# Optimization experiments

Measured on AMD Instinct MI355X. Metric: run time of the kernel, lower is better.

Reference implementation:

```python
import jax, jax.numpy as jnp
import numpy as np

N_NODES = 100000
N_EDGES = 3200000
IN_C = 256
HID = 32
OUT_C = 64


def setup_inputs() -> dict:
    key = jax.random.key(0)
    ks = jax.random.split(key, 12)
    x = jax.random.normal(ks[0], (N_NODES, IN_C), dtype=jnp.float32)
    edge_index = jax.random.randint(ks[1], (2, N_EDGES), 0, N_NODES, dtype=jnp.int64)

    def lin(kw, kb, fan_in, fan_out):
        bound = 1.0 / np.sqrt(fan_in)
        W = jax.random.uniform(kw, (fan_out, fan_in), jnp.float32, -bound, bound)
        b = jax.random.uniform(kb, (fan_out,), jnp.float32, -bound, bound)
        return W, b

    W0, b0 = lin(ks[2], ks[3], IN_C, HID)
    W1, b1 = lin(ks[4], ks[5], HID, HID)
    W2, b2 = lin(ks[6], ks[7], HID, HID)
    W3, b3 = lin(ks[8], ks[9], HID, HID)
    W4, b4 = lin(ks[10], ks[11], HID, OUT_C)
    return {"x": x, "edge_index": edge_index,
            "W0": W0, "b0": b0, "W1": W1, "b1": b1, "W2": W2, "b2": b2,
            "W3": W3, "b3": b3, "W4": W4, "b4": b4}


def _gcn_norm(edge_index, num_nodes):
    # add self loops, symmetric normalization (PyG gcn_norm, edge_weight = 1)
    loop = jnp.arange(num_nodes, dtype=edge_index.dtype)
    row = jnp.concatenate([edge_index[0], loop])  # source nodes
    col = jnp.concatenate([edge_index[1], loop])  # target nodes
    deg = jax.ops.segment_sum(jnp.ones_like(col, dtype=jnp.float32), col,
                              num_segments=num_nodes)
    dinv = jnp.where(deg > 0, jax.lax.rsqrt(jnp.maximum(deg, 1e-12)), 0.0)
    norm = dinv[row] * dinv[col]
    return row, col, norm


def reference(x, edge_index, W0, b0, W1, b1, W2, b2, W3, b3, W4, b4):
    row, col, norm = _gcn_norm(edge_index, N_NODES)

    def prop(h):
        # gather source features, scale by norm, scatter-add to targets
        return jax.ops.segment_sum(norm[:, None] * h[row], col,
                                   num_segments=N_NODES)

    def sgconv(h, W, b):  # SGConv with K=1: propagate then linear
        return prop(h) @ W.T + b

    h = x @ W0.T + b0
    h = jax.nn.relu(sgconv(h, W1, b1))
    h = jax.nn.relu(sgconv(h, W2, b2))
    h = jax.nn.relu(sgconv(h, W3, b3))
    return h @ W4.T + b4
```

## Files before the change

kernel.cpp:

```cpp
#include <hip/hip_runtime.h>
#include <hip/hip_fp16.h>

#define N_NODES 100000
#define N_EDGES 3200000
#define IN_C 256
#define HID 32
#define OUT_C 64
#define CAP 80
#define NP 100032
#define BINW 256
#define BSH 8
#define NBIN 391
#define BCHUNK 8192

typedef _Float16 f16x8 __attribute__((ext_vector_type(8)));
typedef float f32x4 __attribute__((ext_vector_type(4)));

__device__ __forceinline__ float dot4(const float4 a, const float4 b) {
    return a.x * b.x + a.y * b.y + a.z * b.z + a.w * b.w;
}

__device__ __forceinline__ float4 h4tof4(uint2 v) {
    __half2 a = *reinterpret_cast<__half2*>(&v.x);
    __half2 b = *reinterpret_cast<__half2*>(&v.y);
    float2 fa = __half22float2(a), fb = __half22float2(b);
    return make_float4(fa.x, fa.y, fb.x, fb.y);
}
__device__ __forceinline__ uint2 f4toh4(float4 f) {
    __half2 a = __float22half2_rn(make_float2(f.x, f.y));
    __half2 b = __float22half2_rn(make_float2(f.z, f.w));
    uint2 v;
    v.x = *reinterpret_cast<unsigned int*>(&a);
    v.y = *reinterpret_cast<unsigned int*>(&b);
    return v;
}

__device__ __forceinline__ void h8acc(uint4 v, float* acc) {
    __half2* p = reinterpret_cast<__half2*>(&v);
    #pragma unroll
    for (int i = 0; i < 4; ++i) {
        float2 f = __half22float2(p[i]);
        acc[2 * i] += f.x;
        acc[2 * i + 1] += f.y;
    }
}

__device__ __forceinline__ unsigned packh2(_Float16 a, _Float16 b) {
    unsigned short ua = __builtin_bit_cast(unsigned short, a);
    unsigned short ub = __builtin_bit_cast(unsigned short, b);
    return (unsigned)ua | ((unsigned)ub << 16);
}


__global__ __launch_bounds__(256) void k_binhist(const int* __restrict__ col,
                                                 int* __restrict__ binCnt) {
    __shared__ int h[NBIN];
    const int t = threadIdx.x;
    for (int i = t; i < NBIN; i += 256) h[i] = 0;
    __syncthreads();
    const long e0 = (long)blockIdx.x * BCHUNK;
    const long e1 = min((long)N_EDGES, e0 + BCHUNK);
    for (long i = e0 + t; i < e1; i += 256)
        atomicAdd(&h[col[i] >> BSH], 1);
    __syncthreads();
    for (int i = t; i < NBIN; i += 256)
        if (h[i]) atomicAdd(&binCnt[i], h[i]);
}

__global__ void k_binscan(const int* __restrict__ binCnt,
                          int* __restrict__ binStart, int* __restrict__ binCursor) {
    __shared__ int buf[2][512];
    const int t = threadIdx.x;
    int v = (t < NBIN) ? binCnt[t] : 0;
    buf[0][t] = v;
    __syncthreads();
    int s = 0;
    for (int off = 1; off < 512; off <<= 1) {
        int d = s ^ 1;
        int val = buf[s][t];
        if (t >= off) val += buf[s][t - off];
        buf[d][t] = val;
        __syncthreads();
        s = d;
    }
    if (t < NBIN) {
        int st = buf[s][t] - v;
        binStart[t] = st;
        binCursor[t] = st;
    }
}

__global__ __launch_bounds__(256) void k_binscatter(const int* __restrict__ row,
                                                    const int* __restrict__ col,
                                                    int* __restrict__ binCursor,
                                                    int2* __restrict__ pairs) {
    __shared__ int cnt[NBIN];
    __shared__ int ofs[NBIN];
    const int t = threadIdx.x;
    for (int i = t; i < NBIN; i += 256) cnt[i] = 0;
    __syncthreads();
    const long e0 = (long)blockIdx.x * BCHUNK;
    const long e1 = min((long)N_EDGES, e0 + BCHUNK);
    for (long i = e0 + t; i < e1; i += 256)
        atomicAdd(&cnt[col[i] >> BSH], 1);
    __syncthreads();
    for (int i = t; i < NBIN; i += 256) {
        int c = cnt[i];
        ofs[i] = c ? atomicAdd(&binCursor[i], c) : 0;
        cnt[i] = 0;
    }
    __syncthreads();
    for (long i = e0 + t; i < e1; i += 256) {
        int c = col[i];
        int b = c >> BSH;
        int p = ofs[b] + atomicAdd(&cnt[b], 1);
        pairs[p] = make_int2(row[i], c);
    }
}

__global__ __launch_bounds__(256) void k_binbuild(const int2* __restrict__ pairs,
                                                  const int* __restrict__ binStart,
                                                  const int* __restrict__ binCnt,
                                                  int* __restrict__ bucket,
                                                  int* __restrict__ degc,
                                                  float* __restrict__ dinv) {
    __shared__ int cur[BINW];
    const int t = threadIdx.x;
    const int bin = blockIdx.x;
    const int base = bin * BINW;
    cur[t] = 0;
    __syncthreads();
    const int s = binStart[bin], cn = binCnt[bin];
    for (int i = t; i < cn; i += 256) {
        int2 e = pairs[s + i];
        int c = e.y - base;
        int pos = atomicAdd(&cur[c], 1);
        if (pos < CAP) bucket[(size_t)(base + c) * CAP + pos] = e.x;
    }
    __syncthreads();
    int n = base + t;
    if (n < N_NODES) {
        int d = cur[t];
        degc[n] = d;
        dinv[n] = 1.0f / sqrtf((float)(d + 1));
    }
}


__global__ void k_hist(const int* __restrict__ col, int* __restrict__ deg) {
    int i = blockIdx.x * 256 + threadIdx.x;
    if (i < N_EDGES) atomicAdd(&deg[col[i]], 1);
}

__global__ void k_scan1(const int* __restrict__ deg, int* __restrict__ rowptr,
                        int* __restrict__ bsum) {
    __shared__ int buf[2][1024];
    const int t = threadIdx.x, b = blockIdx.x;
    const int i = b * 1024 + t;
    int v = (i < N_NODES) ? deg[i] : 0;
    buf[0][t] = v;
    __syncthreads();
    int src = 0;
    for (int off = 1; off < 1024; off <<= 1) {
        int dst = src ^ 1;
        int val = buf[src][t];
        if (t >= off) val += buf[src][t - off];
        buf[dst][t] = val;
        __syncthreads();
        src = dst;
    }
    int incl = buf[src][t];
    if (i < N_NODES) rowptr[i] = incl - v;
    if (t == 1023) bsum[b] = incl;
}

__global__ void k_scan2(int* __restrict__ bsum, int nb) {
    __shared__ int buf[2][128];
    const int t = threadIdx.x;
    int v = (t < nb) ? bsum[t] : 0;
    buf[0][t] = v;
    __syncthreads();
    int src = 0;
    for (int off = 1; off < 128; off <<= 1) {
        int dst = src ^ 1;
        int val = buf[src][t];
        if (t >= off) val += buf[src][t - off];
        buf[dst][t] = val;
        __syncthreads();
        src = dst;
    }
    if (t < nb) bsum[t] = buf[src][t] - v;
}

__global__ void k_scan3(int* __restrict__ rowptr, const int* __restrict__ bsum) {
    int i = blockIdx.x * 256 + threadIdx.x;
    if (i < N_NODES) rowptr[i] += bsum[i >> 10];
}

__global__ void k_dinv(const int* __restrict__ cnt, int stride,
                       float* __restrict__ dinv, int* __restrict__ degc) {
    int i = blockIdx.x * 256 + threadIdx.x;
    if (i < N_NODES) {
        int d = cnt[i * stride];
        degc[i] = d;
        dinv[i] = 1.0f / sqrtf((float)(d + 1));
    }
}

__global__ void k_scatter(const int* __restrict__ row, const int* __restrict__ col,
                          const int* __restrict__ rowptr, int* __restrict__ cursor,
                          int* __restrict__ csr) {
    int i = blockIdx.x * 256 + threadIdx.x;
    if (i < N_EDGES) {
        int c = col[i];
        int pos = rowptr[c] + atomicAdd(&cursor[c], 1);
        csr[pos] = row[i];
    }
}

__global__ __launch_bounds__(256) void k_lin0_mfma(
        const float* __restrict__ x,
        const float* __restrict__ W0,
        const float* __restrict__ b0,
        const float* __restrict__ dinv,
        uint2* __restrict__ g2) {
    __shared__ f16x8 WH[1024];
    __shared__ f16x8 WL[1024];

    const int t = threadIdx.x;
    const int w = t >> 6;
    const int l = t & 63;
    const int lr = l & 15;
    const int lg = l >> 4;

    for (int s = t; s < 1024; s += 256) {
        const int lane = s & 63;
        const int mtks = s >> 6;
        const int ks = mtks & 7, mt = mtks >> 3;
        const float* wr = W0 + (size_t)(mt * 16 + (lane & 15)) * IN_C
                             + ks * 32 + (lane >> 4) * 8;
        float4 a0 = *(const float4*)(wr);
        float4 a1 = *(const float4*)(wr + 4);
        float v[8] = {a0.x, a0.y, a0.z, a0.w, a1.x, a1.y, a1.z, a1.w};
        f16x8 h, lo;
        #pragma unroll
        for (int e = 0; e < 8; ++e) {
            float sv = v[e] * 16.0f;
            _Float16 hh = (_Float16)sv;
            h[e] = hh;
            lo[e] = (_Float16)(sv - (float)hh);
        }
        WH[s] = h;
        WL[s] = lo;
    }
    __syncthreads();

    const int unit = blockIdx.x * 4 + w;
    if (unit * 32 >= N_NODES) return;
    const int n0 = unit * 32;

    f32x4 acc[2][2];
    #pragma unroll
    for (int mt = 0; mt < 2; ++mt)
        #pragma unroll
        for (int nt = 0; nt < 2; ++nt)
            acc[mt][nt] = (f32x4){0.f, 0.f, 0.f, 0.f};

    const float* xr0 = x + (size_t)(n0 + lr) * IN_C + lg * 8;
    const float* xr1 = x + (size_t)(n0 + 16 + lr) * IN_C + lg * 8;

    #pragma unroll
    for (int ks = 0; ks < 8; ++ks) {
        float4 u0 = *(const float4*)(xr0 + ks * 32);
        float4 u1 = *(const float4*)(xr0 + ks * 32 + 4);
        float4 v0 = *(const float4*)(xr1 + ks * 32);
        float4 v1 = *(const float4*)(xr1 + ks * 32 + 4);
        float fu[8] = {u0.x, u0.y, u0.z, u0.w, u1.x, u1.y, u1.z, u1.w};
        float fv[8] = {v0.x, v0.y, v0.z, v0.w, v1.x, v1.y, v1.z, v1.w};
        f16x8 xh0, xl0, xh1, xl1;
        #pragma unroll
        for (int e = 0; e < 8; ++e) {
            _Float16 h0 = (_Float16)fu[e];
            xh0[e] = h0;
            xl0[e] = (_Float16)(fu[e] - (float)h0);
            _Float16 h1 = (_Float16)fv[e];
            xh1[e] = h1;
            xl1[e] = (_Float16)(fv[e] - (float)h1);
        }
        #pragma unroll
        for (int mt = 0; mt < 2; ++mt) {
            f16x8 wh = WH[mt * 512 + ks * 64 + l];
            f16x8 wl = WL[mt * 512 + ks * 64 + l];
            acc[mt][0] = __builtin_amdgcn_mfma_f32_16x16x32_f16(wh, xh0, acc[mt][0], 0, 0, 0);
            acc[mt][0] = __builtin_amdgcn_mfma_f32_16x16x32_f16(wh, xl0, acc[mt][0], 0, 0, 0);
            acc[mt][0] = __builtin_amdgcn_mfma_f32_16x16x32_f16(wl, xh0, acc[mt][0], 0, 0, 0);
            acc[mt][1] = __builtin_amdgcn_mfma_f32_16x16x32_f16(wh, xh1, acc[mt][1], 0, 0, 0);
            acc[mt][1] = __builtin_amdgcn_mfma_f32_16x16x32_f16(wh, xl1, acc[mt][1], 0, 0, 0);
            acc[mt][1] = __builtin_amdgcn_mfma_f32_16x16x32_f16(wl, xh1, acc[mt][1], 0, 0, 0);
        }
    }

    #pragma unroll
    for (int nt = 0; nt < 2; ++nt) {
        const int node = n0 + nt * 16 + lr;
        const float dv = dinv[node];
        #pragma unroll
        for (int mt = 0; mt < 2; ++mt) {
            const float4 bb = *(const float4*)(b0 + mt * 16 + lg * 4);
            f32x4 a = acc[mt][nt];
            float4 r = make_float4((a[0] * 0.0625f + bb.x) * dv,
                                   (a[1] * 0.0625f + bb.y) * dv,
                                   (a[2] * 0.0625f + bb.z) * dv,
                                   (a[3] * 0.0625f + bb.w) * dv);
            g2[(size_t)node * 8 + mt * 4 + lg] = f4toh4(r);
        }
    }
}

__global__ __launch_bounds__(256) void k_prop_mfma(
        const uint2* __restrict__ g2, const int* __restrict__ idx,
        const int* __restrict__ cnt_arr,
        const float* __restrict__ dinv,
        const float* __restrict__ W, const float* __restrict__ b,
        uint2* __restrict__ gout2) {
    __shared__ f16x8 WH[128], WL[128];
    const int t = threadIdx.x;
    if (t < 128) {
        const int lane = t & 63, mt = t >> 6;
        const float* wr = W + (size_t)(mt * 16 + (lane & 15)) * HID + (lane >> 4) * 8;
        f16x8 h, lo;
        #pragma unroll
        for (int e = 0; e < 8; ++e) {
            float sv = wr[e] * 8.0f;
            _Float16 hh = (_Float16)sv;
            h[e] = hh;
            lo[e] = (_Float16)(sv - (float)hh);
        }
        WH[t] = h;
        WL[t] = lo;
    }
    __syncthreads();

    const int l = t & 63;
    const int tile = blockIdx.x * 4 + (t >> 6);
    const int n0 = tile * 16;
    if (n0 >= N_NODES) return;
    const int node = n0 + (l & 15);
    const int lg = l >> 4;

    const uint4* __restrict__ g4 = (const uint4*)g2;
    float acc[8];
    #pragma unroll
    for (int i = 0; i < 8; ++i) acc[i] = 0.f;
    h8acc(g4[(size_t)node * 4 + lg], acc);

    const int cn = min(cnt_arr[node], CAP);
    const int* __restrict__ e = idx + (size_t)node * CAP;
    int j = 0;
    for (; j + 8 <= cn; j += 8) {
        int4 ra = *(const int4*)(e + j);
        int4 rb = *(const int4*)(e + j + 4);
        uint4 v0 = g4[(size_t)ra.x * 4 + lg];
        uint4 v1 = g4[(size_t)ra.y * 4 + lg];
        uint4 v2 = g4[(size_t)ra.z * 4 + lg];
        uint4 v3 = g4[(size_t)ra.w * 4 + lg];
        uint4 v4 = g4[(size_t)rb.x * 4 + lg];
        uint4 v5 = g4[(size_t)rb.y * 4 + lg];
        uint4 v6 = g4[(size_t)rb.z * 4 + lg];
        uint4 v7 = g4[(size_t)rb.w * 4 + lg];
        h8acc(v0, acc); h8acc(v1, acc); h8acc(v2, acc); h8acc(v3, acc);
        h8acc(v4, acc); h8acc(v5, acc); h8acc(v6, acc); h8acc(v7, acc);
    }
    for (; j < cn; ++j) h8acc(g4[(size_t)e[j] * 4 + lg], acc);

    f16x8 bh, bl;
    #pragma unroll
    for (int i = 0; i < 8; ++i) {
        _Float16 hh = (_Float16)acc[i];
        bh[i] = hh;
        bl[i] = (_Float16)(acc[i] - (float)hh);
    }

    f32x4 c0 = (f32x4){0.f, 0.f, 0.f, 0.f};
    f32x4 c1 = (f32x4){0.f, 0.f, 0.f, 0.f};
    {
        f16x8 wh0 = WH[l], wl0 = WL[l];
        f16x8 wh1 = WH[64 + l], wl1 = WL[64 + l];
        c0 = __builtin_amdgcn_mfma_f32_16x16x32_f16(wh0, bh, c0, 0, 0, 0);
        c0 = __builtin_amdgcn_mfma_f32_16x16x32_f16(wh0, bl, c0, 0, 0, 0);
        c0 = __builtin_amdgcn_mfma_f32_16x16x32_f16(wl0, bh, c0, 0, 0, 0);
        c1 = __builtin_amdgcn_mfma_f32_16x16x32_f16(wh1, bh, c1, 0, 0, 0);
        c1 = __builtin_amdgcn_mfma_f32_16x16x32_f16(wh1, bl, c1, 0, 0, 0);
        c1 = __builtin_amdgcn_mfma_f32_16x16x32_f16(wl1, bh, c1, 0, 0, 0);
    }

    const float dv = dinv[node];
    #pragma unroll
    for (int mt = 0; mt < 2; ++mt) {
        const f32x4 bb = *(const f32x4*)(b + mt * 16 + lg * 4);
        f32x4 a = mt ? c1 : c0;
        float4 r;
        r.x = fmaxf(bb[0] + dv * (a[0] * 0.125f), 0.f) * dv;
        r.y = fmaxf(bb[1] + dv * (a[1] * 0.125f), 0.f) * dv;
        r.z = fmaxf(bb[2] + dv * (a[2] * 0.125f), 0.f) * dv;
        r.w = fmaxf(bb[3] + dv * (a[3] * 0.125f), 0.f) * dv;
        gout2[(size_t)node * 8 + mt * 4 + lg] = f4toh4(r);
    }
}

__global__ __launch_bounds__(256) void k_last_mfma(
        const uint2* __restrict__ g2, const int* __restrict__ idx,
        const int* __restrict__ cnt_arr,
        const float* __restrict__ dinv,
        const float* __restrict__ W3, const float* __restrict__ b3,
        const float* __restrict__ W4, const float* __restrict__ b4,
        float4* __restrict__ out4) {
    __shared__ f16x8 WH3[128], WL3[128];
    __shared__ f16x8 WH4[256], WL4[256];
    const int t = threadIdx.x;
    if (t < 128) {
        const int lane = t & 63, mt = t >> 6;
        const float* wr = W3 + (size_t)(mt * 16 + (lane & 15)) * HID + (lane >> 4) * 8;
        f16x8 h, lo;
        #pragma unroll
        for (int e = 0; e < 8; ++e) {
            float sv = wr[e] * 8.0f;
            _Float16 hh = (_Float16)sv;
            h[e] = hh;
            lo[e] = (_Float16)(sv - (float)hh);
        }
        WH3[t] = h;
        WL3[t] = lo;
    }
    {
        const int lane = t & 63, mt = t >> 6;
        const float* wr = W4 + (size_t)(mt * 16 + (lane & 15)) * HID + (lane >> 4) * 8;
        f16x8 h, lo;
        #pragma unroll
        for (int e = 0; e < 8; ++e) {
            float sv = wr[e] * 8.0f;
            _Float16 hh = (_Float16)sv;
            h[e] = hh;
            lo[e] = (_Float16)(sv - (float)hh);
        }
        WH4[t] = h;
        WL4[t] = lo;
    }
    __syncthreads();

    const int l = t & 63;
    const int tile = blockIdx.x * 4 + (t >> 6);
    const int n0 = tile * 16;
    if (n0 >= N_NODES) return;
    const int nl = l & 15;
    const int node = n0 + nl;
    const int lg = l >> 4;

    const uint4* __restrict__ g4 = (const uint4*)g2;
    float acc[8];
    #pragma unroll
    for (int i = 0; i < 8; ++i) acc[i] = 0.f;
    h8acc(g4[(size_t)node * 4 + lg], acc);

    const int cn = min(cnt_arr[node], CAP);
    const int* __restrict__ e = idx + (size_t)node * CAP;
    int j = 0;
    for (; j + 8 <= cn; j += 8) {
        int4 ra = *(const int4*)(e + j);
        int4 rb = *(const int4*)(e + j + 4);
        uint4 v0 = g4[(size_t)ra.x * 4 + lg];
        uint4 v1 = g4[(size_t)ra.y * 4 + lg];
        uint4 v2 = g4[(size_t)ra.z * 4 + lg];
        uint4 v3 = g4[(size_t)ra.w * 4 + lg];
        uint4 v4 = g4[(size_t)rb.x * 4 + lg];
        uint4 v5 = g4[(size_t)rb.y * 4 + lg];
        uint4 v6 = g4[(size_t)rb.z * 4 + lg];
        uint4 v7 = g4[(size_t)rb.w * 4 + lg];
        h8acc(v0, acc); h8acc(v1, acc); h8acc(v2, acc); h8acc(v3, acc);
        h8acc(v4, acc); h8acc(v5, acc); h8acc(v6, acc); h8acc(v7, acc);
    }
    for (; j < cn; ++j) h8acc(g4[(size_t)e[j] * 4 + lg], acc);

    f16x8 bh, bl;
    #pragma unroll
    for (int i = 0; i < 8; ++i) {
        _Float16 hh = (_Float16)acc[i];
        bh[i] = hh;
        bl[i] = (_Float16)(acc[i] - (float)hh);
    }

    f32x4 c0 = (f32x4){0.f, 0.f, 0.f, 0.f};
    f32x4 c1 = (f32x4){0.f, 0.f, 0.f, 0.f};
    {
        f16x8 wh0 = WH3[l], wl0 = WL3[l];
        f16x8 wh1 = WH3[64 + l], wl1 = WL3[64 + l];
        c0 = __builtin_amdgcn_mfma_f32_16x16x32_f16(wh0, bh, c0, 0, 0, 0);
        c0 = __builtin_amdgcn_mfma_f32_16x16x32_f16(wh0, bl, c0, 0, 0, 0);
        c0 = __builtin_amdgcn_mfma_f32_16x16x32_f16(wl0, bh, c0, 0, 0, 0);
        c1 = __builtin_amdgcn_mfma_f32_16x16x32_f16(wh1, bh, c1, 0, 0, 0);
        c1 = __builtin_amdgcn_mfma_f32_16x16x32_f16(wh1, bl, c1, 0, 0, 0);
        c1 = __builtin_amdgcn_mfma_f32_16x16x32_f16(wl1, bh, c1, 0, 0, 0);
    }

    const float dv = dinv[node];
    const f32x4 b3a = *(const f32x4*)(b3 + lg * 4);
    const f32x4 b3b = *(const f32x4*)(b3 + 16 + lg * 4);
    float h0[4], h1[4];
    #pragma unroll
    for (int r = 0; r < 4; ++r) {
        h0[r] = fmaxf(b3a[r] + dv * (c0[r] * 0.125f), 0.f);
        h1[r] = fmaxf(b3b[r] + dv * (c1[r] * 0.125f), 0.f);
    }

    unsigned ph[2][2], pl_[2][2];
    #pragma unroll
    for (int p = 0; p < 2; ++p) {
        _Float16 a0 = (_Float16)h0[2 * p], a1 = (_Float16)h0[2 * p + 1];
        _Float16 l0 = (_Float16)(h0[2 * p] - (float)a0);
        _Float16 l1 = (_Float16)(h0[2 * p + 1] - (float)a1);
        ph[0][p] = packh2(a0, a1);
        pl_[0][p] = packh2(l0, l1);
        _Float16 c0_ = (_Float16)h1[2 * p], c1_ = (_Float16)h1[2 * p + 1];
        _Float16 d0 = (_Float16)(h1[2 * p] - (float)c0_);
        _Float16 d1 = (_Float16)(h1[2 * p + 1] - (float)c1_);
        ph[1][p] = packh2(c0_, c1_);
        pl_[1][p] = packh2(d0, d1);
    }

    union { unsigned u[4]; f16x8 v; } Bh, Bl;
    #pragma unroll
    for (int q = 0; q < 4; ++q) {
        int src = nl + 16 * ((lg & 1) * 2 + (q >> 1));
        unsigned a0 = (unsigned)__shfl((int)ph[0][q & 1], src, 64);
        unsigned a1 = (unsigned)__shfl((int)ph[1][q & 1], src, 64);
        Bh.u[q] = (lg >= 2) ? a1 : a0;
        unsigned c0_ = (unsigned)__shfl((int)pl_[0][q & 1], src, 64);
        unsigned c1_ = (unsigned)__shfl((int)pl_[1][q & 1], src, 64);
        Bl.u[q] = (lg >= 2) ? c1_ : c0_;
    }

    f32x4 o0 = (f32x4){0.f, 0.f, 0.f, 0.f};
    f32x4 o1 = (f32x4){0.f, 0.f, 0.f, 0.f};
    f32x4 o2 = (f32x4){0.f, 0.f, 0.f, 0.f};
    f32x4 o3 = (f32x4){0.f, 0.f, 0.f, 0.f};
    {
        f16x8 wh, wl;
        wh = WH4[l];        wl = WL4[l];
        o0 = __builtin_amdgcn_mfma_f32_16x16x32_f16(wh, Bh.v, o0, 0, 0, 0);
        o0 = __builtin_amdgcn_mfma_f32_16x16x32_f16(wh, Bl.v, o0, 0, 0, 0);
        o0 = __builtin_amdgcn_mfma_f32_16x16x32_f16(wl, Bh.v, o0, 0, 0, 0);
        wh = WH4[64 + l];   wl = WL4[64 + l];
        o1 = __builtin_amdgcn_mfma_f32_16x16x32_f16(wh, Bh.v, o1, 0, 0, 0);
        o1 = __builtin_amdgcn_mfma_f32_16x16x32_f16(wh, Bl.v, o1, 0, 0, 0);
        o1 = __builtin_amdgcn_mfma_f32_16x16x32_f16(wl, Bh.v, o1, 0, 0, 0);
        wh = WH4[128 + l];  wl = WL4[128 + l];
        o2 = __builtin_amdgcn_mfma_f32_16x16x32_f16(wh, Bh.v, o2, 0, 0, 0);
        o2 = __builtin_amdgcn_mfma_f32_16x16x32_f16(wh, Bl.v, o2, 0, 0, 0);
        o2 = __builtin_amdgcn_mfma_f32_16x16x32_f16(wl, Bh.v, o2, 0, 0, 0);
        wh = WH4[192 + l];  wl = WL4[192 + l];
        o3 = __builtin_amdgcn_mfma_f32_16x16x32_f16(wh, Bh.v, o3, 0, 0, 0);
        o3 = __builtin_amdgcn_mfma_f32_16x16x32_f16(wh, Bl.v, o3, 0, 0, 0);
        o3 = __builtin_amdgcn_mfma_f32_16x16x32_f16(wl, Bh.v, o3, 0, 0, 0);
    }

    #pragma unroll
    for (int mt = 0; mt < 4; ++mt) {
        const f32x4 bb = *(const f32x4*)(b4 + mt * 16 + lg * 4);
        f32x4 a = (mt == 0) ? o0 : (mt == 1) ? o1 : (mt == 2) ? o2 : o3;
        out4[(size_t)node * 16 + mt * 4 + lg] =
            make_float4(a[0] * 0.125f + bb[0], a[1] * 0.125f + bb[1],
                        a[2] * 0.125f + bb[2], a[3] * 0.125f + bb[3]);
    }
}


__global__ __launch_bounds__(256) void k_prop2(
        const uint2* __restrict__ g2, const int* __restrict__ idx,
        const int* __restrict__ base_arr,
        const int* __restrict__ cnt_arr, int maxcnt,
        const float* __restrict__ dinv,
        const float* __restrict__ W, const float* __restrict__ b,
        uint2* __restrict__ gout2) {
    __shared__ float4 Ws[HID * 9];
    const int t = threadIdx.x;
    { int c = t >> 3, k4 = t & 7; Ws[c * 9 + k4] = ((const float4*)W)[t]; }
    __syncthreads();

    const int l = t & 7;
    const int n = blockIdx.x * 32 + (t >> 3);
    if (n >= N_NODES) return;

    int cnt = cnt_arr[n];
    if (cnt > maxcnt) cnt = maxcnt;
    const int base = base_arr ? base_arr[n] : n * CAP;
    const int* __restrict__ e = idx + base;

    float4 acc = h4tof4(g2[n * 8 + l]);
    int j = 0;
    for (; j + 8 <= cnt; j += 8) {
        int r0 = e[j], r1 = e[j + 1], r2 = e[j + 2], r3 = e[j + 3];
        int r4 = e[j + 4], r5 = e[j + 5], r6 = e[j + 6], r7 = e[j + 7];
        uint2 v0 = g2[r0 * 8 + l], v1 = g2[r1 * 8 + l];
        uint2 v2 = g2[r2 * 8 + l], v3 = g2[r3 * 8 + l];
        uint2 v4 = g2[r4 * 8 + l], v5 = g2[r5 * 8 + l];
        uint2 v6 = g2[r6 * 8 + l], v7 = g2[r7 * 8 + l];
        float4 a0 = h4tof4(v0), a1 = h4tof4(v1), a2 = h4tof4(v2), a3 = h4tof4(v3);
        float4 a4 = h4tof4(v4), a5 = h4tof4(v5), a6 = h4tof4(v6), a7 = h4tof4(v7);
        acc.x += a0.x + a1.x + a2.x + a3.x + a4.x + a5.x + a6.x + a7.x;
        acc.y += a0.y + a1.y + a2.y + a3.y + a4.y + a5.y + a6.y + a7.y;
        acc.z += a0.z + a1.z + a2.z + a3.z + a4.z + a5.z + a6.z + a7.z;
        acc.w += a0.w + a1.w + a2.w + a3.w + a4.w + a5.w + a6.w + a7.w;
    }
    for (; j < cnt; ++j) {
        float4 a = h4tof4(g2[e[j] * 8 + l]);
        acc.x += a.x; acc.y += a.y; acc.z += a.z; acc.w += a.w;
    }

    const float dv = dinv[n];
    float4 y = make_float4(0.f, 0.f, 0.f, 0.f);
    #pragma unroll
    for (int m = 0; m < 8; ++m) {
        float4 sv;
        sv.x = __shfl(acc.x, m, 8);
        sv.y = __shfl(acc.y, m, 8);
        sv.z = __shfl(acc.z, m, 8);
        sv.w = __shfl(acc.w, m, 8);
        y.x += dot4(Ws[(4 * l + 0) * 9 + m], sv);
        y.y += dot4(Ws[(4 * l + 1) * 9 + m], sv);
        y.z += dot4(Ws[(4 * l + 2) * 9 + m], sv);
        y.w += dot4(Ws[(4 * l + 3) * 9 + m], sv);
    }
    const float4 bb = ((const float4*)b)[l];
    y.x = fmaxf(bb.x + dv * y.x, 0.f) * dv;
    y.y = fmaxf(bb.y + dv * y.y, 0.f) * dv;
    y.z = fmaxf(bb.z + dv * y.z, 0.f) * dv;
    y.w = fmaxf(bb.w + dv * y.w, 0.f) * dv;
    gout2[n * 8 + l] = f4toh4(y);
}

__global__ __launch_bounds__(256) void k_last2(
        const uint2* __restrict__ g2, const int* __restrict__ idx,
        const int* __restrict__ base_arr,
        const int* __restrict__ cnt_arr, int maxcnt,
        const float* __restrict__ dinv,
        const float* __restrict__ W3, const float* __restrict__ b3,
        const float* __restrict__ W4, const float* __restrict__ b4,
        float4* __restrict__ out4) {
    __shared__ float4 W3s[HID * 9];
    __shared__ float4 W4s[OUT_C * 9];
    const int t = threadIdx.x;
    { int c = t >> 3, k4 = t & 7; W3s[c * 9 + k4] = ((const float4*)W3)[t]; }
    #pragma unroll
    for (int f = t; f < 512; f += 256) {
        int c = f >> 3, k4 = f & 7;
        W4s[c * 9 + k4] = ((const float4*)W4)[f];
    }
    __syncthreads();

    const int l = t & 7;
    const int n = blockIdx.x * 32 + (t >> 3);
    if (n >= N_NODES) return;

    int cnt = cnt_arr[n];
    if (cnt > maxcnt) cnt = maxcnt;
    const int base = base_arr ? base_arr[n] : n * CAP;
    const int* __restrict__ e = idx + base;

    float4 acc = h4tof4(g2[n * 8 + l]);
    int j = 0;
    for (; j + 8 <= cnt; j += 8) {
        int r0 = e[j], r1 = e[j + 1], r2 = e[j + 2], r3 = e[j + 3];
        int r4 = e[j + 4], r5 = e[j + 5], r6 = e[j + 6], r7 = e[j + 7];
        uint2 v0 = g2[r0 * 8 + l], v1 = g2[r1 * 8 + l];
        uint2 v2 = g2[r2 * 8 + l], v3 = g2[r3 * 8 + l];
        uint2 v4 = g2[r4 * 8 + l], v5 = g2[r5 * 8 + l];
        uint2 v6 = g2[r6 * 8 + l], v7 = g2[r7 * 8 + l];
        float4 a0 = h4tof4(v0), a1 = h4tof4(v1), a2 = h4tof4(v2), a3 = h4tof4(v3);
        float4 a4 = h4tof4(v4), a5 = h4tof4(v5), a6 = h4tof4(v6), a7 = h4tof4(v7);
        acc.x += a0.x + a1.x + a2.x + a3.x + a4.x + a5.x + a6.x + a7.x;
        acc.y += a0.y + a1.y + a2.y + a3.y + a4.y + a5.y + a6.y + a7.y;
        acc.z += a0.z + a1.z + a2.z + a3.z + a4.z + a5.z + a6.z + a7.z;
        acc.w += a0.w + a1.w + a2.w + a3.w + a4.w + a5.w + a6.w + a7.w;
    }
    for (; j < cnt; ++j) {
        float4 a = h4tof4(g2[e[j] * 8 + l]);
        acc.x += a.x; acc.y += a.y; acc.z += a.z; acc.w += a.w;
    }

    const float dv = dinv[n];
    float4 y = make_float4(0.f, 0.f, 0.f, 0.f);
    #pragma unroll
    for (int m = 0; m < 8; ++m) {
        float4 sv;
        sv.x = __shfl(acc.x, m, 8);
        sv.y = __shfl(acc.y, m, 8);
        sv.z = __shfl(acc.z, m, 8);
        sv.w = __shfl(acc.w, m, 8);
        y.x += dot4(W3s[(4 * l + 0) * 9 + m], sv);
        y.y += dot4(W3s[(4 * l + 1) * 9 + m], sv);
        y.z += dot4(W3s[(4 * l + 2) * 9 + m], sv);
        y.w += dot4(W3s[(4 * l + 3) * 9 + m], sv);
    }
    const float4 b3v = ((const float4*)b3)[l];
    float4 h;
    h.x = fmaxf(b3v.x + dv * y.x, 0.f);
    h.y = fmaxf(b3v.y + dv * y.y, 0.f);
    h.z = fmaxf(b3v.z + dv * y.z, 0.f);
    h.w = fmaxf(b3v.w + dv * y.w, 0.f);

    float4 ya = make_float4(0.f, 0.f, 0.f, 0.f);
    float4 yb = make_float4(0.f, 0.f, 0.f, 0.f);
    #pragma unroll
    for (int m = 0; m < 8; ++m) {
        float4 hv;
        hv.x = __shfl(h.x, m, 8);
        hv.y = __shfl(h.y, m, 8);
        hv.z = __shfl(h.z, m, 8);
        hv.w = __shfl(h.w, m, 8);
        ya.x += dot4(W4s[(4 * l + 0) * 9 + m], hv);
        ya.y += dot4(W4s[(4 * l + 1) * 9 + m], hv);
        ya.z += dot4(W4s[(4 * l + 2) * 9 + m], hv);
        ya.w += dot4(W4s[(4 * l + 3) * 9 + m], hv);
        yb.x += dot4(W4s[(32 + 4 * l + 0) * 9 + m], hv);
        yb.y += dot4(W4s[(32 + 4 * l + 1) * 9 + m], hv);
        yb.z += dot4(W4s[(32 + 4 * l + 2) * 9 + m], hv);
        yb.w += dot4(W4s[(32 + 4 * l + 3) * 9 + m], hv);
    }
    const float4 b4a = ((const float4*)b4)[l];
    const float4 b4b = ((const float4*)b4)[8 + l];
    ya.x += b4a.x; ya.y += b4a.y; ya.z += b4a.z; ya.w += b4a.w;
    yb.x += b4b.x; yb.y += b4b.y; yb.z += b4b.z; yb.w += b4b.w;
    out4[n * 16 + l] = ya;
    out4[n * 16 + 8 + l] = yb;
}


extern "C" void kernel_launch(void* const* d_in, const int* in_sizes, int n_in,
                              void* d_out, int out_size, void* d_ws, size_t ws_size,
                              hipStream_t stream) {
    const float* x   = (const float*)d_in[0];
    const int*   ei  = (const int*)d_in[1];
    const int*   row = ei;
    const int*   col = ei + N_EDGES;
    const float* W0 = (const float*)d_in[2];
    const float* b0 = (const float*)d_in[3];
    const float* W1 = (const float*)d_in[4];
    const float* b1 = (const float*)d_in[5];
    const float* W2 = (const float*)d_in[6];
    const float* b2 = (const float*)d_in[7];
    const float* W3 = (const float*)d_in[8];
    const float* b3 = (const float*)d_in[9];
    const float* W4 = (const float*)d_in[10];
    const float* b4 = (const float*)d_in[11];
    float* out = (float*)d_out;

    const int EB = (N_EDGES + 255) / 256;
    const int NB256 = (N_NODES + 255) / 256;
    const int NB1024 = (N_NODES + 1023) / 1024;
    const int CB = (N_EDGES + BCHUNK - 1) / BCHUNK;
    const int UNITS = (N_NODES + 31) / 32;
    const int LB0 = (UNITS + 3) / 4;
    const int MB = (N_NODES + 63) / 64;
    const int PB2 = (N_NODES + 31) / 32;

    const size_t UNION_BYTES = (size_t)N_EDGES * sizeof(int2);
    const size_t FAST_BYTES =
        (size_t)N_NODES * CAP * 4 + 2ull * NP * 4 + 3ull * 512 * 4 + UNION_BYTES;

    if (ws_size >= FAST_BYTES) {
        int*   bucket    = (int*)d_ws;
        float* dinv      = (float*)(bucket + (size_t)N_NODES * CAP);
        int*   degc      = (int*)(dinv + NP);
        int*   binCnt    = degc + NP;
        int*   binStart  = binCnt + 512;
        int*   binCursor = binStart + 512;
        char*  uni       = (char*)(binCursor + 512);
        int2*  pairs     = (int2*)uni;
        uint2* gA        = (uint2*)uni;
        uint2* gB        = gA + (size_t)N_NODES * 8;

        hipMemsetAsync(binCnt, 0, 512 * sizeof(int), stream);
        k_binhist<<<CB, 256, 0, stream>>>(col, binCnt);
        k_binscan<<<1, 512, 0, stream>>>(binCnt, binStart, binCursor);
        k_binscatter<<<CB, 256, 0, stream>>>(row, col, binCursor, pairs);
        k_binbuild<<<NBIN, 256, 0, stream>>>(pairs, binStart, binCnt,
                                             bucket, degc, dinv);

        k_lin0_mfma<<<LB0, 256, 0, stream>>>(x, W0, b0, dinv, gA);

        k_prop_mfma<<<MB, 256, 0, stream>>>(gA, bucket, degc, dinv, W1, b1, gB);
        k_prop_mfma<<<MB, 256, 0, stream>>>(gB, bucket, degc, dinv, W2, b2, gA);
        k_last_mfma<<<MB, 256, 0, stream>>>(gA, bucket, degc, dinv,
                                            W3, b3, W4, b4, (float4*)out);
    } else {
        int*   deg    = (int*)d_ws;
        int*   rowptr = deg + NP;
        int*   cursor = rowptr + NP;
        int*   bsum   = cursor + NP;
        float* dinv   = (float*)(bsum + 128);
        int*   csr    = (int*)(dinv + NP);
        uint2* gA     = (uint2*)(csr + N_EDGES);
        uint2* gB     = gA + (size_t)N_NODES * 8;

        hipMemsetAsync(deg, 0, (size_t)NP * 3 * sizeof(int), stream);
        k_hist<<<EB, 256, 0, stream>>>(col, deg);
        k_scan1<<<NB1024, 1024, 0, stream>>>(deg, rowptr, bsum);
        k_scan2<<<1, 128, 0, stream>>>(bsum, NB1024);
        k_scan3<<<NB256, 256, 0, stream>>>(rowptr, bsum);
        k_dinv<<<NB256, 256, 0, stream>>>(deg, 1, dinv, cursor);
        hipMemsetAsync(cursor, 0, (size_t)NP * sizeof(int), stream);
        k_scatter<<<EB, 256, 0, stream>>>(row, col, rowptr, cursor, csr);

        k_lin0_mfma<<<LB0, 256, 0, stream>>>(x, W0, b0, dinv, gA);

        k_prop2<<<PB2, 256, 0, stream>>>(gA, csr, rowptr, deg, 1 << 30,
                                         dinv, W1, b1, gB);
        k_prop2<<<PB2, 256, 0, stream>>>(gB, csr, rowptr, deg, 1 << 30,
                                         dinv, W2, b2, gA);
        k_last2<<<PB2, 256, 0, stream>>>(gA, csr, rowptr, deg, 1 << 30,
                                         dinv, W3, b3, W4, b4, (float4*)out);
    }
}
```

Baseline: 452.9 us.

## Stage binned edges in LDS and pack row/col into one 32-bit word

```diff
diff --git a/kernel.cpp b/kernel.cpp
--- a/kernel.cpp
+++ b/kernel.cpp
@@ -58,9 +58,9 @@
     const int t = threadIdx.x;
     for (int i = t; i < NBIN; i += 256) h[i] = 0;
     __syncthreads();
-    const long e0 = (long)blockIdx.x * BCHUNK;
-    const long e1 = min((long)N_EDGES, e0 + BCHUNK);
-    for (long i = e0 + t; i < e1; i += 256)
+    const int e0 = blockIdx.x * BCHUNK;
+    const int e1 = min(N_EDGES, e0 + BCHUNK);
+    for (int i = e0 + t; i < e1; i += 256)
         atomicAdd(&h[col[i] >> BSH], 1);
     __syncthreads();
     for (int i = t; i < NBIN; i += 256)
@@ -93,32 +93,65 @@
 __global__ __launch_bounds__(256) void k_binscatter(const int* __restrict__ row,
                                                     const int* __restrict__ col,
                                                     int* __restrict__ binCursor,
-                                                    int2* __restrict__ pairs) {
-    __shared__ int cnt[NBIN];
-    __shared__ int ofs[NBIN];
-    const int t = threadIdx.x;
-    for (int i = t; i < NBIN; i += 256) cnt[i] = 0;
-    __syncthreads();
-    const long e0 = (long)blockIdx.x * BCHUNK;
-    const long e1 = min((long)N_EDGES, e0 + BCHUNK);
-    for (long i = e0 + t; i < e1; i += 256)
-        atomicAdd(&cnt[col[i] >> BSH], 1);
-    __syncthreads();
-    for (int i = t; i < NBIN; i += 256) {
-        int c = cnt[i];
-        ofs[i] = c ? atomicAdd(&binCursor[i], c) : 0;
-        cnt[i] = 0;
-    }
-    __syncthreads();
-    for (long i = e0 + t; i < e1; i += 256) {
-        int c = col[i];
-        int b = c >> BSH;
-        int p = ofs[b] + atomicAdd(&cnt[b], 1);
-        pairs[p] = make_int2(row[i], c);
-    }
-}
-
-__global__ __launch_bounds__(256) void k_binbuild(const int2* __restrict__ pairs,
+                                                    unsigned* __restrict__ pairs) {
+    __shared__ int lcnt[512];
+    __shared__ int lofs[512];
+    __shared__ int gbase[512];
+    __shared__ int sbuf[2][256];
+    __shared__ unsigned stage[BCHUNK];
+    __shared__ unsigned short sbin[BCHUNK];
+    const int t = threadIdx.x;
+    for (int i = t; i < 512; i += 256) lcnt[i] = 0;
+    __syncthreads();
+
+    const int e0 = blockIdx.x * BCHUNK;
+    const int e1 = min(N_EDGES, e0 + BCHUNK);
+    const int cn = e1 - e0;
+
+    for (int i = e0 + t; i < e1; i += 256)
+        atomicAdd(&lcnt[col[i] >> BSH], 1);
+    __syncthreads();
+
+    const int a0 = lcnt[2 * t], a1 = lcnt[2 * t + 1];
+    sbuf[0][t] = a0 + a1;
+    __syncthreads();
+    int s = 0;
+    for (int off = 1; off < 256; off <<= 1) {
+        int d = s ^ 1;
+        int v = sbuf[s][t];
+        if (t >= off) v += sbuf[s][t - off];
+        sbuf[d][t] = v;
+        __syncthreads();
+        s = d;
+    }
+    const int excl = sbuf[s][t] - (a0 + a1);
+    lofs[2 * t] = excl;
+    lofs[2 * t + 1] = excl + a0;
+    __syncthreads();
+
+    for (int i = t; i < 512; i += 256) {
+        int c = lcnt[i];
+        gbase[i] = c ? atomicAdd(&binCursor[i], c) : 0;
+        lcnt[i] = 0;
+    }
+    __syncthreads();
+
+    for (int i = e0 + t; i < e1; i += 256) {
+        int cc = col[i];
+        int b = cc >> BSH;
+        int p = lofs[b] + atomicAdd(&lcnt[b], 1);
+        stage[p] = ((unsigned)row[i] << 8) | (unsigned)(cc & 255);
+        sbin[p] = (unsigned short)b;
+    }
+    __syncthreads();
+
+    for (int i = t; i < cn; i += 256) {
+        int b = sbin[i];
+        pairs[gbase[b] + (i - lofs[b])] = stage[i];
+    }
+}
+
+__global__ __launch_bounds__(256) void k_binbuild(const unsigned* __restrict__ pairs,
                                                   const int* __restrict__ binStart,
                                                   const int* __restrict__ binCnt,
                                                   int* __restrict__ bucket,
@@ -132,10 +165,10 @@
     __syncthreads();
     const int s = binStart[bin], cn = binCnt[bin];
     for (int i = t; i < cn; i += 256) {
-        int2 e = pairs[s + i];
-        int c = e.y - base;
+        unsigned p = pairs[s + i];
+        int c = (int)(p & 255u);
         int pos = atomicAdd(&cur[c], 1);
-        if (pos < CAP) bucket[(size_t)(base + c) * CAP + pos] = e.x;
+        if (pos < CAP) bucket[(size_t)(base + c) * CAP + pos] = (int)(p >> 8);
     }
     __syncthreads();
     int n = base + t;
@@ -775,7 +808,7 @@
         int*   binStart  = binCnt + 512;
         int*   binCursor = binStart + 512;
         char*  uni       = (char*)(binCursor + 512);
-        int2*  pairs     = (int2*)uni;
+        unsigned* pairs  = (unsigned*)uni;
         uint2* gA        = (uint2*)uni;
         uint2* gB        = gA + (size_t)N_NODES * 8;
 
```

Measured after the change: 429.9 us. 5.1% less time.
